# Kernel optimization log

Hardware: AMD Instinct MI355X
Metric: run time of the kernel (lower is better)

The kernel has to match this reference:

```python
import jax, jax.numpy as jnp
import numpy as np

B = 128
VOCAB = 32000
EMB = 256
HID = 1024  # units*2 with units=512


def gru_step(x, h, Wi, Wr, bi, br):
    # Keras GRU, reset_after=True, gate order [z, r, h]
    gi = x @ Wi + bi          # [B, 3H]
    gr = h @ Wr + br          # [B, 3H]
    iz, ir, ih = jnp.split(gi, 3, axis=-1)
    rz, rr, rh = jnp.split(gr, 3, axis=-1)
    z = jax.nn.sigmoid(iz + rz)
    r = jax.nn.sigmoid(ir + rr)
    hh = jnp.tanh(ih + r * rh)
    return z * h + (1.0 - z) * hh


def setup_inputs() -> dict:
    key = jax.random.key(0)
    ks = jax.random.split(key, 16)
    s = 0.02
    inp = {
        "x": jax.random.randint(ks[0], (B, 1), 0, VOCAB),
        "h0": jax.random.normal(ks[1], (B, HID), jnp.float32),
        "h1": jax.random.normal(ks[2], (B, HID), jnp.float32),
        "emb": jax.random.normal(ks[3], (VOCAB, EMB), jnp.float32) * s,
        "Wi0": jax.random.normal(ks[4], (EMB, 3 * HID), jnp.float32) * s,
        "Wr0": jax.random.normal(ks[5], (HID, 3 * HID), jnp.float32) * s,
        "bi0": jnp.zeros((3 * HID,), jnp.float32),
        "br0": jnp.zeros((3 * HID,), jnp.float32),
        "Wi1": jax.random.normal(ks[6], (HID, 3 * HID), jnp.float32) * s,
        "Wr1": jax.random.normal(ks[7], (HID, 3 * HID), jnp.float32) * s,
        "bi1": jnp.zeros((3 * HID,), jnp.float32),
        "br1": jnp.zeros((3 * HID,), jnp.float32),
        "ffW": jax.random.normal(ks[8], (HID, VOCAB), jnp.float32) * s,
        "ffb": jnp.zeros((VOCAB,), jnp.float32),
    }
    return inp


def reference(x, h0, h1, emb, Wi0, Wr0, bi0, br0, Wi1, Wr1, bi1, br1, ffW, ffb):
    e = emb[x[:, 0]]                       # [B, EMB] (seq_len == 1)
    h0n = gru_step(e, h0, Wi0, Wr0, bi0, br0)   # [B, H]
    h1n = gru_step(h0n, h1, Wi1, Wr1, bi1, br1)  # [B, H]
    logits = h1n @ ffW + ffb               # [B, VOCAB]
    return logits, h0n, h1n
```

## Files before the change

kernel.cpp:

```cpp
#include <hip/hip_runtime.h>

#define HIDN 1024
#define G3 3072
#define NVOCAB 32000

typedef __bf16 bf16x8 __attribute__((ext_vector_type(8)));
typedef float f32x4 __attribute__((ext_vector_type(4)));
typedef unsigned short ushort4v __attribute__((ext_vector_type(4)));

__device__ __forceinline__ unsigned short f2bf(float f) {
  union { float f; unsigned int u; } v; v.f = f;
  unsigned int u = v.u;
  return (unsigned short)((u + 0x7fffu + ((u >> 16) & 1u)) >> 16);
}

__device__ __forceinline__ float sigmoidf_(float x) {
  return 1.0f / (1.0f + __expf(-x));
}

__device__ __forceinline__ void gload16(const void* g, void* l) {
  __builtin_amdgcn_global_load_lds(
      (const __attribute__((address_space(1))) unsigned int*)g,
      (__attribute__((address_space(3))) unsigned int*)l, 16, 0, 0);
}

__device__ __forceinline__ void gemm_rows(
    const unsigned short* __restrict__ A, int lda, int k0, int Kh,
    const float* __restrict__ W, int ldw, int n0,
    const float* __restrict__ bias, float* __restrict__ C, int ldc,
    char* smem) {
  const int t = threadIdx.x;
  const int w = t >> 6, lane = t & 63;
  const int l15 = lane & 15, kg = lane >> 4;

  f32x4 acc[8];
#pragma unroll
  for (int r = 0; r < 8; ++r) acc[r] = (f32x4)0.0f;

  size_t srcB[2], srcA[2];
#pragma unroll
  for (int m = 0; m < 2; ++m) {
    int g = (w * 2 + m) * 64 + lane;
    {
      int r = g >> 4, q = g & 15;
      int p = q ^ (((r >> 3) & 1) << 2);
      srcB[m] = (size_t)r * ldw + n0 + p * 4;
    }
    {
      int row = g >> 2, uq = g & 3;
      int up = uq ^ ((row >> 1) & 3);
      srcA[m] = (size_t)row * lda + up * 8;
    }
  }

  auto stage = [&](int c, int sel) {
    char* bb = smem + sel * 8192;
    char* ab = smem + 16384 + sel * 8192;
    int kbase = k0 + c * 32;
#pragma unroll
    for (int m = 0; m < 2; ++m)
      gload16(W + (size_t)kbase * ldw + srcB[m], bb + (w * 2 + m) * 1024);
#pragma unroll
    for (int m = 0; m < 2; ++m)
      gload16(A + srcA[m] + kbase, ab + (w * 2 + m) * 1024);
  };

  stage(0, 0);
  __syncthreads();

  const int NC = Kh >> 5;
  const int cl = w * 16 + l15;
  for (int c = 0; c < NC; ++c) {
    int sel = c & 1;
    if (c + 1 < NC) stage(c + 1, sel ^ 1);

    const float* bbf = (const float*)(smem + sel * 8192);
    const unsigned short* abf =
        (const unsigned short*)(smem + 16384 + sel * 8192);

    bf16x8 bfr;
#pragma unroll
    for (int j = 0; j < 8; ++j) {
      int r = kg * 8 + j;
      int q = (cl >> 2) ^ (((r >> 3) & 1) << 2);
      bfr[j] = (__bf16)bbf[r * 64 + q * 4 + (cl & 3)];
    }
#pragma unroll
    for (int rt = 0; rt < 8; ++rt) {
      int row = rt * 16 + l15;
      bf16x8 af =
          *(const bf16x8*)(abf + row * 32 + ((kg ^ ((row >> 1) & 3)) << 3));
      acc[rt] =
          __builtin_amdgcn_mfma_f32_16x16x32_bf16(af, bfr, acc[rt], 0, 0, 0);
    }
    __syncthreads();
  }

  const int col = n0 + cl;
  const float bs = bias ? bias[col] : 0.0f;
#pragma unroll
  for (int rt = 0; rt < 8; ++rt) {
    int rb = rt * 16 + kg * 4;
#pragma unroll
    for (int j = 0; j < 4; ++j)
      C[(size_t)(rb + j) * ldc + col] = acc[rt][j] + bs;
  }
}

__global__ __launch_bounds__(256) void prep_kernel(
    const float* __restrict__ h0, const float* __restrict__ h1,
    const float* __restrict__ emb, const int* __restrict__ x,
    ushort4v* __restrict__ h0b, ushort4v* __restrict__ h1b,
    ushort4v* __restrict__ eb) {
  int i = blockIdx.x * 256 + threadIdx.x;
  float4 v;
  ushort4v* dst;
  if (i < 32768) {
    v = ((const float4*)h0)[i];
    dst = h0b + i;
  } else if (i < 65536) {
    int j = i - 32768;
    v = ((const float4*)h1)[j];
    dst = h1b + j;
  } else {
    int j = i - 65536;
    int b = j >> 6, c = j & 63;
    v = ((const float4*)(emb + (size_t)x[b] * 256))[c];
    dst = eb + j;
  }
  ushort4v o;
  o[0] = f2bf(v.x); o[1] = f2bf(v.y); o[2] = f2bf(v.z); o[3] = f2bf(v.w);
  *dst = o;
}

__global__ __launch_bounds__(256) void gru_gemms_kernel(
    const unsigned short* __restrict__ Xbf, int KX,
    const float* __restrict__ Wi, const float* __restrict__ bi,
    const unsigned short* __restrict__ Hbf,
    const float* __restrict__ Wr, const float* __restrict__ br,
    float* __restrict__ giP, float* __restrict__ grP) {
  __shared__ char smem[32768];
  int bid = blockIdx.x;
  int mat = bid / 96, rem = bid % 96;
  int ks = rem / 48, cb = rem % 48;
  if (mat == 0) {
    int Kh = KX >> 1;
    gemm_rows(Xbf, KX, ks * Kh, Kh, Wi, G3, cb * 64, ks ? nullptr : bi,
              giP + (size_t)ks * 128 * G3, G3, smem);
  } else {
    gemm_rows(Hbf, HIDN, ks * 512, 512, Wr, G3, cb * 64, ks ? nullptr : br,
              grP + (size_t)ks * 128 * G3, G3, smem);
  }
}

__global__ __launch_bounds__(256) void gates_kernel(
    const float* __restrict__ giP, const float* __restrict__ grP,
    const float* __restrict__ hfp, float* __restrict__ hout,
    unsigned short* __restrict__ hbf) {
  int i = blockIdx.x * 256 + threadIdx.x;
  int b = i >> 10, n = i & 1023;
  const float* g0 = giP + (size_t)b * G3;
  const float* g1 = g0 + (size_t)128 * G3;
  const float* r0 = grP + (size_t)b * G3;
  const float* r1 = r0 + (size_t)128 * G3;
  float iz = g0[n] + g1[n], rz = r0[n] + r1[n];
  float ir = g0[1024 + n] + g1[1024 + n], rr = r0[1024 + n] + r1[1024 + n];
  float ih = g0[2048 + n] + g1[2048 + n], rh = r0[2048 + n] + r1[2048 + n];
  float z = sigmoidf_(iz + rz);
  float r = sigmoidf_(ir + rr);
  float hh = tanhf(ih + r * rh);
  float h = hfp[i];
  float o = z * h + (1.0f - z) * hh;
  hout[i] = o;
  hbf[i] = f2bf(o);
}

__global__ __launch_bounds__(256) void ff_kernel(
    const unsigned short* __restrict__ Abf, const float* __restrict__ W,
    const float* __restrict__ bias, float* __restrict__ C) {
  __shared__ char smem[32768];
  gemm_rows(Abf, HIDN, 0, HIDN, W, NVOCAB, blockIdx.x * 64, bias, C, NVOCAB,
            smem);
}

extern "C" void kernel_launch(void* const* d_in, const int* in_sizes, int n_in,
                              void* d_out, int out_size, void* d_ws,
                              size_t ws_size, hipStream_t stream) {
  const int* x = (const int*)d_in[0];
  const float* h0 = (const float*)d_in[1];
  const float* h1 = (const float*)d_in[2];
  const float* emb = (const float*)d_in[3];
  const float* Wi0 = (const float*)d_in[4];
  const float* Wr0 = (const float*)d_in[5];
  const float* bi0 = (const float*)d_in[6];
  const float* br0 = (const float*)d_in[7];
  const float* Wi1 = (const float*)d_in[8];
  const float* Wr1 = (const float*)d_in[9];
  const float* bi1 = (const float*)d_in[10];
  const float* br1 = (const float*)d_in[11];
  const float* ffW = (const float*)d_in[12];
  const float* ffb = (const float*)d_in[13];

  float* out = (float*)d_out;
  float* logits = out;
  float* h0n = out + 4096000;
  float* h1n = out + 4227072;

  unsigned short* h0b = (unsigned short*)d_ws;
  unsigned short* h1b = h0b + 131072;
  unsigned short* eb = h1b + 131072;
  unsigned short* h0nb = eb + 32768;
  unsigned short* h1nb = h0nb + 131072;
  float* giP = (float*)(h1nb + 131072);
  float* grP = giP + 2 * 128 * G3;

  prep_kernel<<<288, 256, 0, stream>>>(h0, h1, emb, x, (ushort4v*)h0b,
                                       (ushort4v*)h1b, (ushort4v*)eb);

  gru_gemms_kernel<<<192, 256, 0, stream>>>(eb, 256, Wi0, bi0, h0b, Wr0, br0,
                                            giP, grP);
  gates_kernel<<<512, 256, 0, stream>>>(giP, grP, h0, h0n, h0nb);

  gru_gemms_kernel<<<192, 256, 0, stream>>>(h0nb, 1024, Wi1, bi1, h1b, Wr1,
                                            br1, giP, grP);
  gates_kernel<<<512, 256, 0, stream>>>(giP, grP, h1, h1n, h1nb);

  ff_kernel<<<500, 256, 0, stream>>>(h1nb, ffW, ffb, logits);
}
```

Measured before the change: 61.81 us.

## Fuse GRU gate GEMMs with activation and triple-buffer FF GEMM

Replaces the split-K GRU GEMM kernel and separate gates kernel with a single fused kernel per layer. Each single-wave block computes a 16x16 output tile for all three gates straight from global memory and applies sigmoid/tanh in registers, so the partial-sum round trip through global memory and two launches are removed. The FF GEMM moves from double to triple buffering in LDS with explicit vmcnt waits and prefetch distance 2. Risks: the fused kernel reads weights directly without LDS staging, and its wave-sized blocks may leave memory parallelism low; the XCD-based tile mapping assumes a particular block placement.

```diff
diff --git a/kernel.cpp b/kernel.cpp
--- a/kernel.cpp
+++ b/kernel.cpp
@@ -22,89 +22,6 @@
   __builtin_amdgcn_global_load_lds(
       (const __attribute__((address_space(1))) unsigned int*)g,
       (__attribute__((address_space(3))) unsigned int*)l, 16, 0, 0);
-}
-
-__device__ __forceinline__ void gemm_rows(
-    const unsigned short* __restrict__ A, int lda, int k0, int Kh,
-    const float* __restrict__ W, int ldw, int n0,
-    const float* __restrict__ bias, float* __restrict__ C, int ldc,
-    char* smem) {
-  const int t = threadIdx.x;
-  const int w = t >> 6, lane = t & 63;
-  const int l15 = lane & 15, kg = lane >> 4;
-
-  f32x4 acc[8];
-#pragma unroll
-  for (int r = 0; r < 8; ++r) acc[r] = (f32x4)0.0f;
-
-  size_t srcB[2], srcA[2];
-#pragma unroll
-  for (int m = 0; m < 2; ++m) {
-    int g = (w * 2 + m) * 64 + lane;
-    {
-      int r = g >> 4, q = g & 15;
-      int p = q ^ (((r >> 3) & 1) << 2);
-      srcB[m] = (size_t)r * ldw + n0 + p * 4;
-    }
-    {
-      int row = g >> 2, uq = g & 3;
-      int up = uq ^ ((row >> 1) & 3);
-      srcA[m] = (size_t)row * lda + up * 8;
-    }
-  }
-
-  auto stage = [&](int c, int sel) {
-    char* bb = smem + sel * 8192;
-    char* ab = smem + 16384 + sel * 8192;
-    int kbase = k0 + c * 32;
-#pragma unroll
-    for (int m = 0; m < 2; ++m)
-      gload16(W + (size_t)kbase * ldw + srcB[m], bb + (w * 2 + m) * 1024);
-#pragma unroll
-    for (int m = 0; m < 2; ++m)
-      gload16(A + srcA[m] + kbase, ab + (w * 2 + m) * 1024);
-  };
-
-  stage(0, 0);
-  __syncthreads();
-
-  const int NC = Kh >> 5;
-  const int cl = w * 16 + l15;
-  for (int c = 0; c < NC; ++c) {
-    int sel = c & 1;
-    if (c + 1 < NC) stage(c + 1, sel ^ 1);
-
-    const float* bbf = (const float*)(smem + sel * 8192);
-    const unsigned short* abf =
-        (const unsigned short*)(smem + 16384 + sel * 8192);
-
-    bf16x8 bfr;
-#pragma unroll
-    for (int j = 0; j < 8; ++j) {
-      int r = kg * 8 + j;
-      int q = (cl >> 2) ^ (((r >> 3) & 1) << 2);
-      bfr[j] = (__bf16)bbf[r * 64 + q * 4 + (cl & 3)];
-    }
-#pragma unroll
-    for (int rt = 0; rt < 8; ++rt) {
-      int row = rt * 16 + l15;
-      bf16x8 af =
-          *(const bf16x8*)(abf + row * 32 + ((kg ^ ((row >> 1) & 3)) << 3));
-      acc[rt] =
-          __builtin_amdgcn_mfma_f32_16x16x32_bf16(af, bfr, acc[rt], 0, 0, 0);
-    }
-    __syncthreads();
-  }
-
-  const int col = n0 + cl;
-  const float bs = bias ? bias[col] : 0.0f;
-#pragma unroll
-  for (int rt = 0; rt < 8; ++rt) {
-    int rb = rt * 16 + kg * 4;
-#pragma unroll
-    for (int j = 0; j < 4; ++j)
-      C[(size_t)(rb + j) * ldc + col] = acc[rt][j] + bs;
-  }
 }
 
 __global__ __launch_bounds__(256) void prep_kernel(
@@ -133,54 +50,178 @@
   *dst = o;
 }
 
-__global__ __launch_bounds__(256) void gru_gemms_kernel(
-    const unsigned short* __restrict__ Xbf, int KX,
-    const float* __restrict__ Wi, const float* __restrict__ bi,
-    const unsigned short* __restrict__ Hbf,
-    const float* __restrict__ Wr, const float* __restrict__ br,
-    float* __restrict__ giP, float* __restrict__ grP) {
-  __shared__ char smem[32768];
-  int bid = blockIdx.x;
-  int mat = bid / 96, rem = bid % 96;
-  int ks = rem / 48, cb = rem % 48;
-  if (mat == 0) {
-    int Kh = KX >> 1;
-    gemm_rows(Xbf, KX, ks * Kh, Kh, Wi, G3, cb * 64, ks ? nullptr : bi,
-              giP + (size_t)ks * 128 * G3, G3, smem);
-  } else {
-    gemm_rows(Hbf, HIDN, ks * 512, 512, Wr, G3, cb * 64, ks ? nullptr : br,
-              grP + (size_t)ks * 128 * G3, G3, smem);
-  }
-}
-
-__global__ __launch_bounds__(256) void gates_kernel(
-    const float* __restrict__ giP, const float* __restrict__ grP,
-    const float* __restrict__ hfp, float* __restrict__ hout,
+__global__ __launch_bounds__(64) void gru_fused_kernel(
+    const unsigned short* __restrict__ Xb, int KX,
+    const unsigned short* __restrict__ Hb,
+    const float* __restrict__ Wi, const float* __restrict__ Wr,
+    const float* __restrict__ bi, const float* __restrict__ br,
+    const float* __restrict__ hprev, float* __restrict__ hout,
     unsigned short* __restrict__ hbf) {
-  int i = blockIdx.x * 256 + threadIdx.x;
-  int b = i >> 10, n = i & 1023;
-  const float* g0 = giP + (size_t)b * G3;
-  const float* g1 = g0 + (size_t)128 * G3;
-  const float* r0 = grP + (size_t)b * G3;
-  const float* r1 = r0 + (size_t)128 * G3;
-  float iz = g0[n] + g1[n], rz = r0[n] + r1[n];
-  float ir = g0[1024 + n] + g1[1024 + n], rr = r0[1024 + n] + r1[1024 + n];
-  float ih = g0[2048 + n] + g1[2048 + n], rh = r0[2048 + n] + r1[2048 + n];
-  float z = sigmoidf_(iz + rz);
-  float r = sigmoidf_(ir + rr);
-  float hh = tanhf(ih + r * rh);
-  float h = hfp[i];
-  float o = z * h + (1.0f - z) * hh;
-  hout[i] = o;
-  hbf[i] = f2bf(o);
+  const int bid = blockIdx.x;
+  const int xcd = bid & 7, s = bid >> 3;
+  const int cg = xcd * 8 + (s >> 3);
+  const int rg = s & 7;
+  const int n0 = cg * 16, r0 = rg * 16;
+  const int lane = threadIdx.x;
+  const int l15 = lane & 15, kg = lane >> 4;
+
+  f32x4 az = (f32x4)0.0f, ar = (f32x4)0.0f;
+  f32x4 aih = (f32x4)0.0f, arh = (f32x4)0.0f;
+
+  const int NCX = KX >> 5;
+#pragma unroll 2
+  for (int c = 0; c < NCX; ++c) {
+    bf16x8 ax =
+        *(const bf16x8*)(Xb + (size_t)(r0 + l15) * KX + c * 32 + kg * 8);
+    const float* wb = Wi + (size_t)(c * 32 + kg * 8) * G3 + n0 + l15;
+    float v0[8], v1[8], v2[8];
+#pragma unroll
+    for (int j = 0; j < 8; ++j) {
+      const float* wj = wb + (size_t)j * G3;
+      v0[j] = wj[0];
+      v1[j] = wj[1024];
+      v2[j] = wj[2048];
+    }
+    bf16x8 b0, b1, b2;
+#pragma unroll
+    for (int j = 0; j < 8; ++j) {
+      b0[j] = (__bf16)v0[j];
+      b1[j] = (__bf16)v1[j];
+      b2[j] = (__bf16)v2[j];
+    }
+    az = __builtin_amdgcn_mfma_f32_16x16x32_bf16(ax, b0, az, 0, 0, 0);
+    ar = __builtin_amdgcn_mfma_f32_16x16x32_bf16(ax, b1, ar, 0, 0, 0);
+    aih = __builtin_amdgcn_mfma_f32_16x16x32_bf16(ax, b2, aih, 0, 0, 0);
+  }
+
+#pragma unroll 2
+  for (int c = 0; c < 32; ++c) {
+    bf16x8 ah =
+        *(const bf16x8*)(Hb + (size_t)(r0 + l15) * HIDN + c * 32 + kg * 8);
+    const float* wb = Wr + (size_t)(c * 32 + kg * 8) * G3 + n0 + l15;
+    float v0[8], v1[8], v2[8];
+#pragma unroll
+    for (int j = 0; j < 8; ++j) {
+      const float* wj = wb + (size_t)j * G3;
+      v0[j] = wj[0];
+      v1[j] = wj[1024];
+      v2[j] = wj[2048];
+    }
+    bf16x8 b0, b1, b2;
+#pragma unroll
+    for (int j = 0; j < 8; ++j) {
+      b0[j] = (__bf16)v0[j];
+      b1[j] = (__bf16)v1[j];
+      b2[j] = (__bf16)v2[j];
+    }
+    az = __builtin_amdgcn_mfma_f32_16x16x32_bf16(ah, b0, az, 0, 0, 0);
+    ar = __builtin_amdgcn_mfma_f32_16x16x32_bf16(ah, b1, ar, 0, 0, 0);
+    arh = __builtin_amdgcn_mfma_f32_16x16x32_bf16(ah, b2, arh, 0, 0, 0);
+  }
+
+  const int col = n0 + l15;
+  const float bz = bi[col] + br[col];
+  const float brr = bi[1024 + col] + br[1024 + col];
+  const float bih = bi[2048 + col], brh = br[2048 + col];
+#pragma unroll
+  for (int j = 0; j < 4; ++j) {
+    const int row = r0 + kg * 4 + j;
+    float z = sigmoidf_(az[j] + bz);
+    float r = sigmoidf_(ar[j] + brr);
+    float hh = tanhf(aih[j] + bih + r * (arh[j] + brh));
+    float h = hprev[(size_t)row * HIDN + col];
+    float o = z * h + (1.0f - z) * hh;
+    hout[(size_t)row * HIDN + col] = o;
+    hbf[(size_t)row * HIDN + col] = f2bf(o);
+  }
 }
 
 __global__ __launch_bounds__(256) void ff_kernel(
-    const unsigned short* __restrict__ Abf, const float* __restrict__ W,
+    const unsigned short* __restrict__ A, const float* __restrict__ W,
     const float* __restrict__ bias, float* __restrict__ C) {
-  __shared__ char smem[32768];
-  gemm_rows(Abf, HIDN, 0, HIDN, W, NVOCAB, blockIdx.x * 64, bias, C, NVOCAB,
-            smem);
+  __shared__ char smem[49152];
+  const int n0 = blockIdx.x * 64;
+  const int t = threadIdx.x;
+  const int w = t >> 6, lane = t & 63;
+  const int l15 = lane & 15, kg = lane >> 4;
+
+  f32x4 acc[8];
+#pragma unroll
+  for (int r = 0; r < 8; ++r) acc[r] = (f32x4)0.0f;
+
+  size_t srcB[2], srcA[2];
+#pragma unroll
+  for (int m = 0; m < 2; ++m) {
+    int g = (w * 2 + m) * 64 + lane;
+    {
+      int r = g >> 4, q = g & 15;
+      int p = q ^ (((r >> 3) & 1) << 2);
+      srcB[m] = (size_t)r * NVOCAB + n0 + p * 4;
+    }
+    {
+      int row = g >> 2, uq = g & 3;
+      int up = uq ^ ((row >> 1) & 3);
+      srcA[m] = (size_t)row * HIDN + up * 8;
+    }
+  }
+
+  auto stage = [&](int c, int sel) {
+    char* bb = smem + sel * 8192;
+    char* ab = smem + 24576 + sel * 8192;
+    int kbase = c * 32;
+#pragma unroll
+    for (int m = 0; m < 2; ++m)
+      gload16(W + (size_t)kbase * NVOCAB + srcB[m], bb + (w * 2 + m) * 1024);
+#pragma unroll
+    for (int m = 0; m < 2; ++m)
+      gload16(A + srcA[m] + kbase, ab + (w * 2 + m) * 1024);
+  };
+
+  stage(0, 0);
+  stage(1, 1);
+
+  const int NC = HIDN >> 5;
+  const int cl = w * 16 + l15;
+  for (int c = 0; c < NC; ++c) {
+    if (c + 1 < NC)
+      asm volatile("s_waitcnt vmcnt(4)" ::: "memory");
+    else
+      asm volatile("s_waitcnt vmcnt(0)" ::: "memory");
+    __builtin_amdgcn_s_barrier();
+    asm volatile("" ::: "memory");
+
+    int sel = c % 3;
+    const float* bbf = (const float*)(smem + sel * 8192);
+    const unsigned short* abf =
+        (const unsigned short*)(smem + 24576 + sel * 8192);
+
+    bf16x8 bfr;
+#pragma unroll
+    for (int j = 0; j < 8; ++j) {
+      int r = kg * 8 + j;
+      int q = (cl >> 2) ^ (((r >> 3) & 1) << 2);
+      bfr[j] = (__bf16)bbf[r * 64 + q * 4 + (cl & 3)];
+    }
+#pragma unroll
+    for (int rt = 0; rt < 8; ++rt) {
+      int row = rt * 16 + l15;
+      bf16x8 af =
+          *(const bf16x8*)(abf + row * 32 + ((kg ^ ((row >> 1) & 3)) << 3));
+      acc[rt] =
+          __builtin_amdgcn_mfma_f32_16x16x32_bf16(af, bfr, acc[rt], 0, 0, 0);
+    }
+    if (c + 2 < NC) stage(c + 2, (c + 2) % 3);
+  }
+
+  const int col = n0 + cl;
+  const float bs = bias[col];
+#pragma unroll
+  for (int rt = 0; rt < 8; ++rt) {
+    int rb = rt * 16 + kg * 4;
+#pragma unroll
+    for (int j = 0; j < 4; ++j)
+      C[(size_t)(rb + j) * NVOCAB + col] = acc[rt][j] + bs;
+  }
 }
 
 extern "C" void kernel_launch(void* const* d_in, const int* in_sizes, int n_in,
@@ -211,19 +252,15 @@
   unsigned short* eb = h1b + 131072;
   unsigned short* h0nb = eb + 32768;
   unsigned short* h1nb = h0nb + 131072;
-  float* giP = (float*)(h1nb + 131072);
-  float* grP = giP + 2 * 128 * G3;
 
   prep_kernel<<<288, 256, 0, stream>>>(h0, h1, emb, x, (ushort4v*)h0b,
                                        (ushort4v*)h1b, (ushort4v*)eb);
 
-  gru_gemms_kernel<<<192, 256, 0, stream>>>(eb, 256, Wi0, bi0, h0b, Wr0, br0,
-                                            giP, grP);
-  gates_kernel<<<512, 256, 0, stream>>>(giP, grP, h0, h0n, h0nb);
-
-  gru_gemms_kernel<<<192, 256, 0, stream>>>(h0nb, 1024, Wi1, bi1, h1b, Wr1,
-                                            br1, giP, grP);
-  gates_kernel<<<512, 256, 0, stream>>>(giP, grP, h1, h1n, h1nb);
+  gru_fused_kernel<<<512, 64, 0, stream>>>(eb, 256, h0b, Wi0, Wr0, bi0, br0,
+                                           h0, h0n, h0nb);
+
+  gru_fused_kernel<<<512, 64, 0, stream>>>(h0nb, 1024, h1b, Wi1, Wr1, bi1,
+                                           br1, h1, h1n, h1nb);
 
   ff_kernel<<<500, 256, 0, stream>>>(h1nb, ffW, ffb, logits);
 }
```

After: 86.98 us. +40.7%, slower.
